# Kernel tuning notes

Measured on AMD Instinct MI355X. Metric: run time of the kernel, lower is better.

The kernel has to match this reference:

```python
import jax, jax.numpy as jnp
import numpy as np

NINP = 512
NHEAD = 8


def setup_inputs() -> dict:
    key = jax.random.key(0)
    ks = jax.random.split(key, 7)
    B, M, L, C = 2, 32, 512, NINP
    s = 1.0 / np.sqrt(C)
    return {
        "x": jax.random.normal(ks[0], (B, M, L, C), dtype=jnp.float32),
        "Wq": jax.random.normal(ks[1], (C, C), dtype=jnp.float32) * s,
        "bq": jax.random.normal(ks[2], (C,), dtype=jnp.float32) * s,
        "Wk": jax.random.normal(ks[3], (C, C), dtype=jnp.float32) * s,
        "bk": jax.random.normal(ks[4], (C,), dtype=jnp.float32) * s,
        "Wv": jax.random.normal(ks[5], (C, C), dtype=jnp.float32) * s,
        "bv": jax.random.normal(ks[6], (C,), dtype=jnp.float32) * s,
    }


def reference(x, Wq, bq, Wk, bk, Wv, bv) -> jnp.ndarray:
    # x: (B, M, L, C). Attention over L within each (B, M) block.
    B, M, L, C = x.shape
    H = NHEAD
    D = C // H
    scale = 1.0 / jnp.sqrt(jnp.asarray(D, dtype=x.dtype))

    def split_heads(t):  # (B,M,L,C) -> (B,M,H,L,D)
        return t.reshape(B, M, L, H, D).transpose(0, 1, 3, 2, 4)

    q = split_heads(x @ Wq + bq)
    k = split_heads(x @ Wk + bk)
    v = split_heads(x @ Wv + bv)

    scores = jnp.einsum("bmhid,bmhjd->bmhij", q, k) * scale
    w = jax.nn.softmax(scores, axis=-1)  # dropout p=0 -> identity
    out = jnp.einsum("bmhij,bmhjd->bmhid", w, v)  # (B,M,H,L,D)
    return out.transpose(0, 1, 3, 2, 4).reshape(B, M, L, C)
```

## Files before the change

kernel.cpp:

```cpp
#include <hip/hip_runtime.h>


typedef unsigned short u16;
typedef unsigned int u32;
typedef unsigned long long u64;
typedef __bf16 bf16x8 __attribute__((ext_vector_type(8)));
typedef float f32x4 __attribute__((ext_vector_type(4)));

#define SCQ 0.18033688011112042f

static __device__ __forceinline__ u16 f2bf(float f) {
  u32 x = __float_as_uint(f);
  x += 0x7fffu + ((x >> 16) & 1u);
  return (u16)(x >> 16);
}

static __device__ __forceinline__ u32 pkbf(float f0, float f1) {
  return __builtin_amdgcn_perm(__float_as_uint(f1) + 0x8000u,
                               __float_as_uint(f0) + 0x8000u, 0x07060302u);
}

typedef __attribute__((address_space(1))) const void* gvp;
typedef __attribute__((address_space(3))) void* lvp;
static __device__ __forceinline__ void glds16(const void* g, void* l) {
  __builtin_amdgcn_global_load_lds((gvp)g, (lvp)l, 16, 0, 0);
}

__global__ __launch_bounds__(256) void prep(const float* __restrict__ x,
                                            u16* __restrict__ xb,
                                            const float* __restrict__ Wq,
                                            const float* __restrict__ Wk,
                                            const float* __restrict__ Wv,
                                            u16* __restrict__ WT) {
  __shared__ float t[32][33];
  const int bx = blockIdx.x;
  if (bx < 8192) {
    const u32 i = (bx * 256u + threadIdx.x) * 8u;
    const float4 a = *(const float4*)(x + i);
    const float4 b = *(const float4*)(x + i + 4);
    union { u16 r[8]; uint4 v; } u;
    u.r[0] = f2bf(a.x); u.r[1] = f2bf(a.y); u.r[2] = f2bf(a.z); u.r[3] = f2bf(a.w);
    u.r[4] = f2bf(b.x); u.r[5] = f2bf(b.y); u.r[6] = f2bf(b.z); u.r[7] = f2bf(b.w);
    *(uint4*)(xb + i) = u.v;
    return;
  }
  const int b = bx - 8192;
  const int z = b >> 8;
  const int rem = b & 255;
  const float* W = (z == 0) ? Wq : ((z == 1) ? Wk : Wv);
  u16* dst = WT + z * 262144;
  const int k0 = (rem >> 4) * 32, n0 = (rem & 15) * 32;
  const int tx = threadIdx.x & 31, ty = threadIdx.x >> 5;
#pragma unroll
  for (int i = 0; i < 32; i += 8)
    t[ty + i][tx] = W[(size_t)(k0 + ty + i) * 512 + n0 + tx];
  __syncthreads();
#pragma unroll
  for (int i = 0; i < 32; i += 8)
    dst[(size_t)(n0 + ty + i) * 512 + k0 + tx] = f2bf(t[tx][ty + i]);
}

__global__ __launch_bounds__(256) void gemm_qkv(const u16* __restrict__ xb,
                                                const u16* __restrict__ WT,
                                                const float* __restrict__ bq,
                                                const float* __restrict__ bk,
                                                const float* __restrict__ bv,
                                                u16* __restrict__ qkv) {
  __shared__ __align__(16) u16 smem[16384];
  const int z = blockIdx.x >> 2;
  const int nbase = (blockIdx.x & 3) * 128;
  const int mbase = blockIdx.y * 128;
  const u16* Bg = WT + z * 262144;
  const float* bias = (z == 0) ? bq : ((z == 1) ? bk : bv);
  u16* out = qkv + (size_t)z * 16777216u;
  const int tid = threadIdx.x;
  const int lane = tid & 63;
  const int w = tid >> 6;
  const int wy = w >> 1, wx = w & 1;
  const int m15 = lane & 15, g = lane >> 4;

  const int srow = w * 32 + (lane >> 2);
  const int scol = (lane & 3) * 8;
  const u16* Ap = xb + (size_t)(mbase + srow) * 512 + scol;
  const u16* Bp = Bg + (size_t)(nbase + srow) * 512 + scol;

  u16* buf0 = smem;
  u16* buf1 = smem + 8192;

  f32x4 acc[4][4] = {};

#define STAGE(KT, B)                                  \
  do {                                                \
    const int k0_ = (KT) * 32;                        \
    u16* d_ = (B) + w * 1024;                         \
    glds16(Ap + k0_, d_);                             \
    glds16(Ap + k0_ + 16 * 512, d_ + 512);            \
    glds16(Bp + k0_, d_ + 4096);                      \
    glds16(Bp + k0_ + 16 * 512, d_ + 4096 + 512);     \
  } while (0)

#define COMPUTE(B)                                                          \
  do {                                                                      \
    bf16x8 af[4], bfr[4];                                                   \
    _Pragma("unroll") for (int t = 0; t < 4; ++t)                           \
        af[t] = *(const bf16x8*)&(B)[(wy * 64 + t * 16 + m15) * 32 + g * 8];\
    _Pragma("unroll") for (int t = 0; t < 4; ++t)                           \
        bfr[t] = *(const bf16x8*)&(B)[4096 + (wx * 64 + t * 16 + m15) * 32 + g * 8]; \
    _Pragma("unroll") for (int rt = 0; rt < 4; ++rt)                        \
        _Pragma("unroll") for (int ct = 0; ct < 4; ++ct)                    \
            acc[rt][ct] = __builtin_amdgcn_mfma_f32_16x16x32_bf16(          \
                af[rt], bfr[ct], acc[rt][ct], 0, 0, 0);                     \
  } while (0)

  STAGE(0, buf0);
  STAGE(1, buf1);

#pragma unroll
  for (int kt = 0; kt < 16; ++kt) {
    u16* cb = (kt & 1) ? buf1 : buf0;
    if (kt < 15)
      asm volatile("s_waitcnt vmcnt(4)" ::: "memory");
    else
      asm volatile("s_waitcnt vmcnt(0)" ::: "memory");
    __builtin_amdgcn_s_barrier();
    COMPUTE(cb);
    asm volatile("s_waitcnt lgkmcnt(0)" ::: "memory");
    __builtin_amdgcn_s_barrier();
    if (kt + 2 < 16) STAGE(kt + 2, cb);
  }
#undef STAGE
#undef COMPUTE

  if (z < 2) {
    const float sc = (z == 0) ? SCQ : 1.0f;
#pragma unroll
    for (int ct = 0; ct < 4; ++ct) {
      const int col = nbase + wx * 64 + ct * 16 + m15;
      const float bb = bias[col];
#pragma unroll
      for (int rt = 0; rt < 4; ++rt) {
        const int row0 = mbase + wy * 64 + rt * 16 + g * 4;
#pragma unroll
        for (int r = 0; r < 4; ++r)
          out[(size_t)(row0 + r) * 512 + col] = f2bf((acc[rt][ct][r] + bb) * sc);
      }
    }
  } else {
    const int bm = mbase >> 9, jb = mbase & 511;
    u16* sT = smem;
#pragma unroll
    for (int cn = 0; cn < 4; ++cn) {
      __syncthreads();
      if (wx == (cn >> 1)) {
#pragma unroll
        for (int cte = 0; cte < 2; ++cte) {
          const int ct = (cn & 1) * 2 + cte;
          const int ncol = nbase + wx * 64 + ct * 16 + m15;
          const float bb = bias[ncol];
          const int nl = cte * 16 + m15;
#pragma unroll
          for (int rt = 0; rt < 4; ++rt) {
            u64 pk = 0;
#pragma unroll
            for (int r = 0; r < 4; ++r)
              pk |= (u64)f2bf(acc[rt][ct][r] + bb) << (16 * r);
            *(u64*)&sT[nl * 136 + wy * 64 + rt * 16 + g * 4] = pk;
          }
        }
      }
      __syncthreads();
#pragma unroll
      for (int it = 0; it < 2; ++it) {
        const int nl = it * 16 + (tid >> 4);
        const int ml = (tid & 15) * 8;
        const int ng = nbase + cn * 32 + nl;
        const int h = ng >> 6, d = ng & 63;
        *(uint4*)(out + ((size_t)((bm * 8 + h) * 64 + d)) * 512 + jb + ml) =
            *(const uint4*)&sT[nl * 136 + ml];
      }
    }
  }
}

__global__ __launch_bounds__(256) void attn(const u16* __restrict__ Q,
                                            const u16* __restrict__ K,
                                            const u16* __restrict__ Vt,
                                            float* __restrict__ out) {
  __shared__ __align__(16) char smem[36864];
  u16* sK = (u16*)smem;
  u16* sVT = (u16*)(smem + 9216);
  const int tid = threadIdx.x;
  const int lane = tid & 63;
  const int w = tid >> 6;
  const int m15 = lane & 15, g = lane >> 4;
  const int qt = blockIdx.x, h = blockIdx.y, bm = blockIdx.z;
  const size_t rb = (size_t)bm * 512;
  const int q0 = qt * 128 + w * 32;
  u16* sPT = (u16*)(smem + 18432) + w * 2304;

  bf16x8 qf[2][2];
#pragma unroll
  for (int ct = 0; ct < 2; ++ct)
#pragma unroll
    for (int kc = 0; kc < 2; ++kc)
      qf[ct][kc] =
          *(const bf16x8*)(Q + (rb + q0 + ct * 16 + m15) * 512 + h * 64 + kc * 32 + g * 8);

  f32x4 acc[4][2] = {};
  f32x4 lv[2] = {};

  const int srow = tid >> 3, sc8 = (tid & 7) * 8;
  const u16* Kb = K + rb * 512 + h * 64;
  const u16* Vtb = Vt + (size_t)(bm * 8 + h) * 64 * 512;

  uint4 k0v = *(const uint4*)(Kb + (size_t)srow * 512 + sc8);
  uint4 k1v = *(const uint4*)(Kb + (size_t)(srow + 32) * 512 + sc8);
  uint4 v0v = *(const uint4*)(Vtb + (size_t)srow * 512 + sc8);
  uint4 v1v = *(const uint4*)(Vtb + (size_t)(srow + 32) * 512 + sc8);

  for (int jt = 0; jt < 8; ++jt) {
    asm volatile("s_waitcnt lgkmcnt(0)" ::: "memory");
    __builtin_amdgcn_s_barrier();
    asm volatile("s_waitcnt vmcnt(0)" ::: "memory");
    *(uint4*)&sK[srow * 72 + sc8] = k0v;
    *(uint4*)&sK[(srow + 32) * 72 + sc8] = k1v;
    *(uint4*)&sVT[srow * 72 + sc8] = v0v;
    *(uint4*)&sVT[(srow + 32) * 72 + sc8] = v1v;
    if (jt < 7) {
      const int j1 = (jt + 1) * 64;
      k0v = *(const uint4*)(Kb + (size_t)(j1 + srow) * 512 + sc8);
      k1v = *(const uint4*)(Kb + (size_t)(j1 + srow + 32) * 512 + sc8);
      v0v = *(const uint4*)(Vtb + (size_t)srow * 512 + j1 + sc8);
      v1v = *(const uint4*)(Vtb + (size_t)(srow + 32) * 512 + j1 + sc8);
    }
    asm volatile("s_waitcnt lgkmcnt(0)" ::: "memory");
    __builtin_amdgcn_s_barrier();

    f32x4 s[4][2];
#pragma unroll
    for (int rt = 0; rt < 4; ++rt) {
      const bf16x8 k0 = *(const bf16x8*)&sK[(rt * 16 + m15) * 72 + g * 8];
      const bf16x8 k1 = *(const bf16x8*)&sK[(rt * 16 + m15) * 72 + 32 + g * 8];
#pragma unroll
      for (int ct = 0; ct < 2; ++ct) {
        f32x4 z = {};
        z = __builtin_amdgcn_mfma_f32_16x16x32_bf16(k0, qf[ct][0], z, 0, 0, 0);
        s[rt][ct] = __builtin_amdgcn_mfma_f32_16x16x32_bf16(k1, qf[ct][1], z, 0, 0, 0);
      }
    }

#pragma unroll
    for (int ct = 0; ct < 2; ++ct)
#pragma unroll
      for (int rt = 0; rt < 4; ++rt) {
        f32x4 p;
#pragma unroll
        for (int r = 0; r < 4; ++r) p[r] = exp2f(s[rt][ct][r]);
        lv[ct] += p;
        uint2 pk = {pkbf(p[0], p[1]), pkbf(p[2], p[3])};
        *(uint2*)&sPT[(ct * 16 + m15) * 72 + rt * 16 + g * 4] = pk;
      }

    bf16x8 pb[2][2];
#pragma unroll
    for (int ct = 0; ct < 2; ++ct)
#pragma unroll
      for (int kc = 0; kc < 2; ++kc)
        pb[ct][kc] = *(const bf16x8*)&sPT[(ct * 16 + m15) * 72 + kc * 32 + g * 8];
#pragma unroll
    for (int dt = 0; dt < 4; ++dt) {
      const bf16x8 v0 = *(const bf16x8*)&sVT[(dt * 16 + m15) * 72 + g * 8];
      const bf16x8 v1 = *(const bf16x8*)&sVT[(dt * 16 + m15) * 72 + 32 + g * 8];
#pragma unroll
      for (int ct = 0; ct < 2; ++ct) {
        acc[dt][ct] = __builtin_amdgcn_mfma_f32_16x16x32_bf16(v0, pb[ct][0], acc[dt][ct], 0, 0, 0);
        acc[dt][ct] = __builtin_amdgcn_mfma_f32_16x16x32_bf16(v1, pb[ct][1], acc[dt][ct], 0, 0, 0);
      }
    }
  }

  float inv[2];
#pragma unroll
  for (int ct = 0; ct < 2; ++ct) {
    float l = lv[ct][0] + lv[ct][1] + lv[ct][2] + lv[ct][3];
    l += __shfl_xor(l, 16);
    l += __shfl_xor(l, 32);
    inv[ct] = 1.0f / l;
  }
  __syncthreads();
  float* sO = (float*)(smem + w * 4608);
#pragma unroll
  for (int c = 0; c < 2; ++c) {
#pragma unroll
    for (int dt2 = 0; dt2 < 2; ++dt2)
#pragma unroll
      for (int ct = 0; ct < 2; ++ct) {
        f32x4 v = acc[c * 2 + dt2][ct] * inv[ct];
        *(f32x4*)&sO[(ct * 16 + m15) * 36 + dt2 * 16 + g * 4] = v;
      }
#pragma unroll
    for (int it = 0; it < 4; ++it) {
      const int q = it * 8 + (lane >> 3);
      f32x4 v = *(const f32x4*)&sO[q * 36 + (lane & 7) * 4];
      *(f32x4*)&out[(rb + q0 + q) * 512 + h * 64 + c * 32 + (lane & 7) * 4] = v;
    }
  }
}

extern "C" void kernel_launch(void* const* d_in, const int* in_sizes, int n_in,
                              void* d_out, int out_size, void* d_ws, size_t ws_size,
                              hipStream_t stream) {
  const float* x = (const float*)d_in[0];
  const float* Wq = (const float*)d_in[1];
  const float* bq = (const float*)d_in[2];
  const float* Wk = (const float*)d_in[3];
  const float* bk = (const float*)d_in[4];
  const float* Wv = (const float*)d_in[5];
  const float* bv = (const float*)d_in[6];
  float* out = (float*)d_out;

  u16* ws = (u16*)d_ws;
  u16* xb = ws;
  u16* WT = ws + 16777216;
  u16* qkv = ws + 17563648;

  prep<<<8960, 256, 0, stream>>>(x, xb, Wq, Wk, Wv, WT);
  gemm_qkv<<<dim3(12, 256, 1), 256, 0, stream>>>(xb, WT, bq, bk, bv, qkv);
  attn<<<dim3(4, 8, 64), 256, 0, stream>>>(qkv, qkv + 16777216, qkv + 2 * 16777216, out);
}
```

Before: 262.9 us.

## Compute Q, K and V tiles in one block to reuse staged x tiles

The QKV GEMM now has each block compute the matching 128x128 tile for all three projections, loading each x tile into shared memory once and multiplying it against three weight tiles. This removes the threefold reloading of x across separate per-projection blocks. In exchange, shared memory doubles to 64KB, there are three times as many accumulators (48 f32x4 per thread), and the grid shrinks to 1024 blocks, which may reduce occupancy and increase register pressure.

```diff
diff --git a/kernel.cpp b/kernel.cpp
--- a/kernel.cpp
+++ b/kernel.cpp
@@ -66,50 +66,47 @@
                                                 const float* __restrict__ bk,
                                                 const float* __restrict__ bv,
                                                 u16* __restrict__ qkv) {
-  __shared__ __align__(16) u16 smem[16384];
-  const int z = blockIdx.x >> 2;
-  const int nbase = (blockIdx.x & 3) * 128;
-  const int mbase = blockIdx.y * 128;
-  const u16* Bg = WT + z * 262144;
-  const float* bias = (z == 0) ? bq : ((z == 1) ? bk : bv);
-  u16* out = qkv + (size_t)z * 16777216u;
+  __shared__ __align__(16) u16 smem[32768];
   const int tid = threadIdx.x;
   const int lane = tid & 63;
   const int w = tid >> 6;
   const int wy = w >> 1, wx = w & 1;
   const int m15 = lane & 15, g = lane >> 4;
+  const int mbase = blockIdx.x * 128;
+  const int nbase = blockIdx.y * 128;
 
   const int srow = w * 32 + (lane >> 2);
   const int scol = (lane & 3) * 8;
   const u16* Ap = xb + (size_t)(mbase + srow) * 512 + scol;
-  const u16* Bp = Bg + (size_t)(nbase + srow) * 512 + scol;
+  const u16* Bp = WT + (size_t)(nbase + srow) * 512 + scol;
 
   u16* buf0 = smem;
-  u16* buf1 = smem + 8192;
-
-  f32x4 acc[4][4] = {};
-
-#define STAGE(KT, B)                                  \
-  do {                                                \
-    const int k0_ = (KT) * 32;                        \
-    u16* d_ = (B) + w * 1024;                         \
-    glds16(Ap + k0_, d_);                             \
-    glds16(Ap + k0_ + 16 * 512, d_ + 512);            \
-    glds16(Bp + k0_, d_ + 4096);                      \
-    glds16(Bp + k0_ + 16 * 512, d_ + 4096 + 512);     \
+  u16* buf1 = smem + 16384;
+
+  f32x4 accQ[4][4] = {}, accK[4][4] = {}, accV[4][4] = {};
+
+#define STAGE(KT, B)                                         \
+  do {                                                       \
+    const int k0_ = (KT) * 32;                               \
+    u16* da_ = (B) + w * 1024;                               \
+    glds16(Ap + k0_, da_);                                   \
+    glds16(Ap + k0_ + 16 * 512, da_ + 512);                  \
+    _Pragma("unroll") for (int z_ = 0; z_ < 3; ++z_) {       \
+      u16* db_ = (B) + 4096 * (1 + z_) + w * 1024;           \
+      glds16(Bp + z_ * 262144 + k0_, db_);                   \
+      glds16(Bp + z_ * 262144 + k0_ + 16 * 512, db_ + 512);  \
+    }                                                        \
   } while (0)
 
-#define COMPUTE(B)                                                          \
-  do {                                                                      \
-    bf16x8 af[4], bfr[4];                                                   \
-    _Pragma("unroll") for (int t = 0; t < 4; ++t)                           \
-        af[t] = *(const bf16x8*)&(B)[(wy * 64 + t * 16 + m15) * 32 + g * 8];\
-    _Pragma("unroll") for (int t = 0; t < 4; ++t)                           \
-        bfr[t] = *(const bf16x8*)&(B)[4096 + (wx * 64 + t * 16 + m15) * 32 + g * 8]; \
-    _Pragma("unroll") for (int rt = 0; rt < 4; ++rt)                        \
-        _Pragma("unroll") for (int ct = 0; ct < 4; ++ct)                    \
-            acc[rt][ct] = __builtin_amdgcn_mfma_f32_16x16x32_bf16(          \
-                af[rt], bfr[ct], acc[rt][ct], 0, 0, 0);                     \
+#define CZ(ACC, B, ZOFF)                                                          \
+  do {                                                                            \
+    bf16x8 bfr[4];                                                                \
+    _Pragma("unroll") for (int t = 0; t < 4; ++t)                                 \
+        bfr[t] = *(const bf16x8*)&(B)[(ZOFF) + (wx * 64 + t * 16 + m15) * 32 + g * 8]; \
+    _Pragma("unroll") for (int rt = 0; rt < 4; ++rt)                              \
+        _Pragma("unroll") for (int ct = 0; ct < 4; ++ct)                          \
+            ACC[rt][ct] = __builtin_amdgcn_mfma_f32_16x16x32_bf16(                \
+                af[rt], bfr[ct], ACC[rt][ct], 0, 0, 0);                           \
   } while (0)
 
   STAGE(0, buf0);
@@ -119,33 +116,43 @@
   for (int kt = 0; kt < 16; ++kt) {
     u16* cb = (kt & 1) ? buf1 : buf0;
     if (kt < 15)
-      asm volatile("s_waitcnt vmcnt(4)" ::: "memory");
+      asm volatile("s_waitcnt vmcnt(8)" ::: "memory");
     else
       asm volatile("s_waitcnt vmcnt(0)" ::: "memory");
     __builtin_amdgcn_s_barrier();
-    COMPUTE(cb);
+    {
+      bf16x8 af[4];
+#pragma unroll
+      for (int t = 0; t < 4; ++t)
+        af[t] = *(const bf16x8*)&cb[(wy * 64 + t * 16 + m15) * 32 + g * 8];
+      CZ(accQ, cb, 4096);
+      CZ(accK, cb, 8192);
+      CZ(accV, cb, 12288);
+    }
     asm volatile("s_waitcnt lgkmcnt(0)" ::: "memory");
     __builtin_amdgcn_s_barrier();
     if (kt + 2 < 16) STAGE(kt + 2, cb);
   }
 #undef STAGE
-#undef COMPUTE
-
-  if (z < 2) {
-    const float sc = (z == 0) ? SCQ : 1.0f;
-#pragma unroll
-    for (int ct = 0; ct < 4; ++ct) {
-      const int col = nbase + wx * 64 + ct * 16 + m15;
-      const float bb = bias[col];
-#pragma unroll
-      for (int rt = 0; rt < 4; ++rt) {
-        const int row0 = mbase + wy * 64 + rt * 16 + g * 4;
-#pragma unroll
-        for (int r = 0; r < 4; ++r)
-          out[(size_t)(row0 + r) * 512 + col] = f2bf((acc[rt][ct][r] + bb) * sc);
-      }
-    }
-  } else {
+#undef CZ
+
+#pragma unroll
+  for (int ct = 0; ct < 4; ++ct) {
+    const int col = nbase + wx * 64 + ct * 16 + m15;
+    const float bbq = bq[col], bbk = bk[col];
+#pragma unroll
+    for (int rt = 0; rt < 4; ++rt) {
+      const int row0 = mbase + wy * 64 + rt * 16 + g * 4;
+#pragma unroll
+      for (int r = 0; r < 4; ++r) {
+        qkv[(size_t)(row0 + r) * 512 + col] = f2bf((accQ[rt][ct][r] + bbq) * SCQ);
+        qkv[16777216u + (size_t)(row0 + r) * 512 + col] = f2bf(accK[rt][ct][r] + bbk);
+      }
+    }
+  }
+
+  {
+    u16* outV = qkv + 2 * 16777216u;
     const int bm = mbase >> 9, jb = mbase & 511;
     u16* sT = smem;
 #pragma unroll
@@ -156,14 +163,14 @@
         for (int cte = 0; cte < 2; ++cte) {
           const int ct = (cn & 1) * 2 + cte;
           const int ncol = nbase + wx * 64 + ct * 16 + m15;
-          const float bb = bias[ncol];
+          const float bb = bv[ncol];
           const int nl = cte * 16 + m15;
 #pragma unroll
           for (int rt = 0; rt < 4; ++rt) {
             u64 pk = 0;
 #pragma unroll
             for (int r = 0; r < 4; ++r)
-              pk |= (u64)f2bf(acc[rt][ct][r] + bb) << (16 * r);
+              pk |= (u64)f2bf(accV[rt][ct][r] + bb) << (16 * r);
             *(u64*)&sT[nl * 136 + wy * 64 + rt * 16 + g * 4] = pk;
           }
         }
@@ -175,7 +182,7 @@
         const int ml = (tid & 15) * 8;
         const int ng = nbase + cn * 32 + nl;
         const int h = ng >> 6, d = ng & 63;
-        *(uint4*)(out + ((size_t)((bm * 8 + h) * 64 + d)) * 512 + jb + ml) =
+        *(uint4*)(outV + ((size_t)((bm * 8 + h) * 64 + d)) * 512 + jb + ml) =
             *(const uint4*)&sT[nl * 136 + ml];
       }
     }
@@ -325,6 +332,6 @@
   u16* qkv = ws + 17563648;
 
   prep<<<8960, 256, 0, stream>>>(x, xb, Wq, Wk, Wv, WT);
-  gemm_qkv<<<dim3(12, 256, 1), 256, 0, stream>>>(xb, WT, bq, bk, bv, qkv);
+  gemm_qkv<<<dim3(256, 4), 256, 0, stream>>>(xb, WT, bq, bk, bv, qkv);
   attn<<<dim3(4, 8, 64), 256, 0, stream>>>(qkv, qkv + 16777216, qkv + 2 * 16777216, out);
 }
```

After: 278.6 us. 6.0% more time.
